# Optimization experiments

Hardware: AMD Instinct MI355X
Metric: run time of the kernel (lower is better)

## Reference

```python
import jax, jax.numpy as jnp
import numpy as np

N_TRAIN, N_FEAT, N_HID, ENC = 4096, 64, 256, 256
N_ANTES, ATT_H, MAX_LEN = 2048, 256, 16


def setup_inputs() -> dict:
    key = jax.random.key(0)
    ks = jax.random.split(key, 8)
    s = 0.05
    f32 = jnp.float32
    return {
        "context": jax.random.normal(ks[0], (N_TRAIN, N_FEAT), f32),
        "S": jax.random.uniform(ks[1], (N_TRAIN, N_ANTES), dtype=f32),
        "enc_w1": s * jax.random.normal(ks[2], (N_HID, N_FEAT), f32),
        "enc_b1": jnp.zeros((N_HID,), f32),
        "enc_w2": s * jax.random.normal(ks[3], (ENC, N_HID), f32),
        "enc_b2": jnp.zeros((ENC,), f32),
        "w_ih": s * jax.random.normal(ks[4], (4 * ENC, N_ANTES), f32),
        "w_hh": s * jax.random.normal(ks[5], (4 * ENC, ENC), f32),
        "b_ih": jnp.zeros((4 * ENC,), f32),
        "b_hh": jnp.zeros((4 * ENC,), f32),
        "att_w1": s * jax.random.normal(ks[6], (ATT_H, N_TRAIN + ENC), f32),
        "att_b1": jnp.zeros((ATT_H,), f32),
        "att_w2": s * jax.random.normal(ks[7], (1, ATT_H), f32),
        "att_b2": jnp.zeros((1,), f32),
    }


def _forward(context, S, enc_w1, enc_b1, enc_w2, enc_b2,
             w_ih, w_hh, b_ih, b_hh, att_w1, att_b1, att_w2, att_b2):
    n_train, n_antes = S.shape
    # context encoder: Linear -> ReLU -> Linear, initializes LSTM hidden state
    phi = jax.nn.relu(context @ enc_w1.T + enc_b1) @ enc_w2.T + enc_b2  # [n_train, ENC]
    # attention first layer split: columns [:n_train] act on S.T rows, rest on e_t
    Wa, Wb = att_w1[:, :n_train], att_w1[:, n_train:]
    pre = S.T @ Wa.T  # [n_antes, ATT_H], constant across timesteps
    bias = b_ih + b_hh
    x0 = jnp.ones((n_train, n_antes), S.dtype)

    def step(carry, _):
        h, c, x = carry
        # one LSTM cell step (PyTorch gate order i, f, g, o)
        z = x @ w_ih.T + h @ w_hh.T + bias  # [n_train, 4*ENC]
        i, f, g, o = jnp.split(z, 4, axis=-1)
        c = jax.nn.sigmoid(f) * c + jax.nn.sigmoid(i) * jnp.tanh(g)
        h = jax.nn.sigmoid(o) * jnp.tanh(c)
        e_t = h.mean(axis=0)  # mean over n_train (torch e.mean(1) on [1,n_train,H])
        hid = jax.nn.relu(pre + e_t @ Wb.T + att_b1)  # [n_antes, ATT_H]
        scores = (hid @ att_w2.T + att_b2)[:, 0]      # [n_antes]
        logp = jax.nn.log_softmax(scores, axis=0)
        idx = jnp.argmax(logp)
        # next input: chosen antecedent column broadcast across all antecedents
        x_next = jnp.broadcast_to(S[:, idx][:, None], (n_train, n_antes))
        return (h, c, x_next), logp

    _, d = jax.lax.scan(jax.checkpoint(step), (phi, jnp.zeros_like(phi), x0),
                        None, length=MAX_LEN)
    return d  # [MAX_LEN, n_antes] == torch cat(...).transpose(0, 1)


def reference(context, S, enc_w1, enc_b1, enc_w2, enc_b2,
              w_ih, w_hh, b_ih, b_hh, att_w1, att_b1, att_w2, att_b2):
    return _forward(context, S, enc_w1, enc_b1, enc_w2, enc_b2,
                    w_ih, w_hh, b_ih, b_hh, att_w1, att_b1, att_w2, att_b2)
```

## Files before the change

### kernel.cpp

```cpp
#include <hip/hip_runtime.h>
#include <hip/hip_bf16.h>
#include <math.h>

#define N_TRAIN 4096
#define N_FEAT  64
#define N_HID   256
#define ENC     256
#define N_ANTES 2048
#define ATT_H   256
#define MAX_LEN 16

typedef unsigned int u32;
typedef unsigned short u16;
typedef short short8 __attribute__((ext_vector_type(8)));
typedef float floatx16 __attribute__((ext_vector_type(16)));

__device__ __forceinline__ float fsig(float x)  { return 1.f / (1.f + __expf(-x)); }
__device__ __forceinline__ float ftanh(float x) { return 2.f / (1.f + __expf(-2.f * x)) - 1.f; }

__device__ __forceinline__ u16 f2bf(float x) {
    u32 b = __float_as_uint(x);
    return (u16)((b + 0x7FFFu + ((b >> 16) & 1u)) >> 16);
}
__device__ __forceinline__ float bf2f(u16 h) {
    return __uint_as_float(((u32)h) << 16);
}
__device__ __forceinline__ void split_bf(float v, u16& hi, u16& lo) {
    u32 b = __float_as_uint(v);
    hi = (u16)(b >> 16);
    float r = v - __uint_as_float(b & 0xFFFF0000u);
    lo = (u16)(__float_as_uint(r) >> 16);
}

__device__ __forceinline__ int kin_of(int l, int j) {
    return ((l >> 5) << 2) + (j & 3) + ((j >> 2) << 3);
}

template <bool RELU>
__global__ __launch_bounds__(256) void gemm_abT(
    const float* __restrict__ A, const float* __restrict__ B,
    const float* __restrict__ bias, float* __restrict__ C,
    int M, int N, int K, int lda, int ldb, int ldc)
{
    __shared__ __align__(16) float As[16][68];
    __shared__ __align__(16) float Bs[16][68];
    const int tid = threadIdx.x;
    const int m0 = blockIdx.x * 64, n0 = blockIdx.y * 64;
    const int tx = tid & 15, ty = tid >> 4;
    const int kl = tid & 15, rl = tid >> 4;
    float acc[4][4] = {};

    for (int k0 = 0; k0 < K; k0 += 16) {
        #pragma unroll
        for (int pp = 0; pp < 4; ++pp) {
            int r = rl + pp * 16;
            As[kl][r] = A[(size_t)(m0 + r) * lda + k0 + kl];
            Bs[kl][r] = B[(size_t)(n0 + r) * ldb + k0 + kl];
        }
        __syncthreads();
        #pragma unroll
        for (int k = 0; k < 16; ++k) {
            float4 av = *(const float4*)&As[k][ty * 4];
            float4 bv = *(const float4*)&Bs[k][tx * 4];
            float a4[4] = {av.x, av.y, av.z, av.w};
            float b4[4] = {bv.x, bv.y, bv.z, bv.w};
            #pragma unroll
            for (int i = 0; i < 4; ++i)
                #pragma unroll
                for (int j = 0; j < 4; ++j)
                    acc[i][j] = fmaf(a4[i], b4[j], acc[i][j]);
        }
        __syncthreads();
    }
    #pragma unroll
    for (int i = 0; i < 4; ++i) {
        int m = m0 + ty * 4 + i;
        #pragma unroll
        for (int j = 0; j < 4; ++j) {
            int n = n0 + tx * 4 + j;
            float v = acc[i][j] + bias[n];
            if (RELU) v = fmaxf(v, 0.f);
            C[(size_t)m * ldc + n] = v;
        }
    }
}

__global__ __launch_bounds__(256) void k_rowsum(const float* __restrict__ w_ih,
                                                float* __restrict__ rowsum)
{
    __shared__ float red[256];
    const int j = blockIdx.x, tid = threadIdx.x;
    float s = 0.f;
    for (int i = tid; i < N_ANTES; i += 256) s += w_ih[(size_t)j * N_ANTES + i];
    red[tid] = s; __syncthreads();
    for (int off = 128; off > 0; off >>= 1) {
        if (tid < off) red[tid] += red[tid + off];
        __syncthreads();
    }
    if (tid == 0) rowsum[j] = red[0];
}

__global__ __launch_bounds__(256) void k_wbT(const float* __restrict__ att_w1,
                                             float* __restrict__ WbT)
{
    int gid = blockIdx.x * 256 + threadIdx.x;
    int j = gid >> 8, k = gid & 255;
    WbT[(size_t)k * 256 + j] = att_w1[(size_t)j * (N_TRAIN + ENC) + N_TRAIN + k];
}

__global__ __launch_bounds__(256) void k_packAf(const float* __restrict__ att_w1,
                                                u16* __restrict__ Af_hi,
                                                u16* __restrict__ Af_lo)
{
    int gid = blockIdx.x * 256 + threadIdx.x;
    int j  = gid & 7;
    int l  = (gid >> 3) & 63;
    int kt = (gid >> 9) & 255;
    int mt = gid >> 17;
    int m = mt * 32 + (l & 31);
    int k = kt * 16 + kin_of(l, j);
    float v = att_w1[(size_t)m * (N_TRAIN + ENC) + k];
    u16 hi, lo; split_bf(v, hi, lo);
    Af_hi[gid] = hi;
    Af_lo[gid] = lo;
}

#define PSPLIT 8
__global__ __launch_bounds__(256) void k_gemm_preT(
    const u16* __restrict__ Af_hi, const u16* __restrict__ Af_lo,
    const float* __restrict__ S, float* __restrict__ P)
{
    const int tid = threadIdx.x, lane = tid & 63, w = tid >> 6;
    const int kz = blockIdx.x;
    const int np = blockIdx.y;
    const int mq = blockIdx.z;
    const int mt = mq * 2 + (w & 1);
    const int ni = w >> 1;
    const int nb = np * 64 + ni * 32 + (lane & 31);
    const int kb = 4 * (lane >> 5);
    floatx16 acc = {0,0,0,0,0,0,0,0,0,0,0,0,0,0,0,0};

    const int kt_beg = kz * 32, kt_end = kt_beg + 32;
    #pragma unroll 4
    for (int kt = kt_beg; kt < kt_end; ++kt) {
        size_t ao = (((size_t)mt * 256 + kt) * 64 + lane) * 8;
        short8 ahi = *(const short8*)(Af_hi + ao);
        short8 alo = *(const short8*)(Af_lo + ao);
        short8 bhi, blo;
        #pragma unroll
        for (int j = 0; j < 8; ++j) {
            int k = kt * 16 + kb + (j & 3) + 8 * (j >> 2);
            float v = S[(size_t)k * N_ANTES + nb];
            u16 hi, lo; split_bf(v, hi, lo);
            bhi[j] = (short)hi;
            blo[j] = (short)lo;
        }
        acc = __builtin_amdgcn_mfma_f32_32x32x16_bf16(ahi, bhi, acc, 0, 0, 0);
        acc = __builtin_amdgcn_mfma_f32_32x32x16_bf16(ahi, blo, acc, 0, 0, 0);
        acc = __builtin_amdgcn_mfma_f32_32x32x16_bf16(alo, bhi, acc, 0, 0, 0);
    }

    float* Pk = P + (size_t)(kz & 3) * (ATT_H * N_ANTES);
    #pragma unroll
    for (int q = 0; q < 16; ++q) {
        int row = mt * 32 + (q & 3) + 8 * (q >> 2) + 4 * (lane >> 5);
        atomicAdd(&Pk[(size_t)row * N_ANTES + nb], acc[q]);
    }
}

__global__ __launch_bounds__(256) void k_reduce4(const float* __restrict__ P,
                                                 float* __restrict__ preT)
{
    int gid = blockIdx.x * 256 + threadIdx.x;
    const int SZ = ATT_H * N_ANTES;
    preT[gid] = (P[gid] + P[gid + SZ]) + (P[gid + 2 * SZ] + P[gid + 3 * SZ]);
}

__global__ __launch_bounds__(256) void k_packWf(const float* __restrict__ w_hh,
                                                u16* __restrict__ Wf_hi,
                                                u16* __restrict__ Wf_lo)
{
    int gid = blockIdx.x * 256 + threadIdx.x;
    int j    = gid & 7;
    int l    = (gid >> 3) & 63;
    int kt   = (gid >> 9) & 15;
    int nsub = (gid >> 13) & 1;
    int cb   = gid >> 14;
    int k  = kt * 16 + kin_of(l, j);
    int cc = nsub * 32 + (l & 31);
    int jj = cb * 16 + (cc >> 2);
    int g  = cc & 3;
    int J  = g * 256 + jj;
    float v = w_hh[(size_t)J * 256 + k];
    u16 hi = f2bf(v);
    Wf_hi[gid] = hi;
    Wf_lo[gid] = f2bf(v - bf2f(hi));
}

__global__ __launch_bounds__(256) void k_packHf(const float* __restrict__ h,
                                                u16* __restrict__ Hf_hi,
                                                u16* __restrict__ Hf_lo)
{
    int gid = blockIdx.x * 256 + threadIdx.x;
    int j  = gid & 7;
    int l  = (gid >> 3) & 63;
    int kt = (gid >> 9) & 15;
    int mt = gid >> 13;
    int m = mt * 32 + (l & 31);
    int k = kt * 16 + kin_of(l, j);
    float v = h[(size_t)m * 256 + k];
    u16 hi = f2bf(v);
    Hf_hi[gid] = hi;
    Hf_lo[gid] = f2bf(v - bf2f(hi));
}

__global__ __launch_bounds__(256) void k_zgemm(
    const u16* __restrict__ Hf_hi_r, const u16* __restrict__ Hf_lo_r,
    u16* __restrict__ Hf_hi_w, u16* __restrict__ Hf_lo_w,
    const u16* __restrict__ Wf_hi, const u16* __restrict__ Wf_lo,
    float* __restrict__ c,
    const float* __restrict__ rowsum, const float* __restrict__ b_ih,
    const float* __restrict__ b_hh, const float* __restrict__ S,
    const int* __restrict__ idx_buf, int t, float* __restrict__ e_acc_t)
{
    __shared__ __align__(16) float z_lds[64][68];
    __shared__ float red[256];
    const int tid  = threadIdx.x;
    const int lane = tid & 63;
    const int w    = tid >> 6;
    const int rb = blockIdx.x;
    const int cb = blockIdx.y;
    const int mt = rb * 2 + (w & 1);
    const int ni = w >> 1;

    floatx16 acc = {0,0,0,0,0,0,0,0,0,0,0,0,0,0,0,0};
    const size_t aoff = (size_t)mt * 16 * 512 + lane * 8;
    const size_t boff = (size_t)(cb * 2 + ni) * 16 * 512 + lane * 8;

    #pragma unroll 4
    for (int kt = 0; kt < 16; ++kt) {
        short8 ahi = *(const short8*)(Hf_hi_r + aoff + kt * 512);
        short8 alo = *(const short8*)(Hf_lo_r + aoff + kt * 512);
        short8 bhi = *(const short8*)(Wf_hi   + boff + kt * 512);
        short8 blo = *(const short8*)(Wf_lo   + boff + kt * 512);
        acc = __builtin_amdgcn_mfma_f32_32x32x16_bf16(ahi, bhi, acc, 0, 0, 0);
        acc = __builtin_amdgcn_mfma_f32_32x32x16_bf16(ahi, blo, acc, 0, 0, 0);
        acc = __builtin_amdgcn_mfma_f32_32x32x16_bf16(alo, bhi, acc, 0, 0, 0);
    }

    #pragma unroll
    for (int q = 0; q < 16; ++q) {
        int row = (w & 1) * 32 + (q & 3) + 8 * (q >> 2) + 4 * (lane >> 5);
        z_lds[row][ni * 32 + (lane & 31)] = acc[q];
    }
    __syncthreads();

    const int jj_l = tid & 15, rg = tid >> 4;
    const int Jc = cb * 16 + jj_l;
    float rs[4], bs[4];
    #pragma unroll
    for (int g = 0; g < 4; ++g) {
        int J = g * 256 + Jc;
        rs[g] = rowsum[J];
        bs[g] = b_ih[J] + b_hh[J];
    }
    const int idxp = (t > 0) ? idx_buf[t - 1] : 0;
    float esum = 0.f;
    #pragma unroll
    for (int p = 0; p < 4; ++p) {
        int r = rg * 4 + p;
        int rglob = rb * 64 + r;
        float a = (t > 0) ? S[(size_t)rglob * N_ANTES + idxp] : 1.f;
        float4 z4 = *(const float4*)&z_lds[r][jj_l * 4];
        float zi = z4.x + fmaf(a, rs[0], bs[0]);
        float zf = z4.y + fmaf(a, rs[1], bs[1]);
        float zg = z4.z + fmaf(a, rs[2], bs[2]);
        float zo = z4.w + fmaf(a, rs[3], bs[3]);
        size_t coff = (size_t)rglob * 256 + Jc;
        float cn = fsig(zf) * c[coff] + fsig(zi) * ftanh(zg);
        float hn = fsig(zo) * ftanh(cn);
        c[coff] = cn;
        esum += hn;
        u16 hi = f2bf(hn);
        u16 lo = f2bf(hn - bf2f(hi));
        int mtw    = rglob >> 5;
        int lane_a = (rglob & 31) + 32 * ((Jc >> 2) & 1);
        int ktw    = Jc >> 4;
        int jw     = (Jc & 3) + ((Jc >> 3) & 1) * 4;
        size_t off = (((size_t)mtw * 16 + ktw) * 64 + lane_a) * 8 + jw;
        Hf_hi_w[off] = hi;
        Hf_lo_w[off] = lo;
    }
    red[tid] = esum;
    __syncthreads();
    if (tid < 16) {
        float s = 0.f;
        #pragma unroll
        for (int q = 0; q < 16; ++q) s += red[tid + q * 16];
        atomicAdd(&e_acc_t[Jc - jj_l + tid], s);
    }
}

__global__ __launch_bounds__(256) void k_att(
    const float* __restrict__ preT, const float* __restrict__ e_accum_t,
    const float* __restrict__ WbT, const float* __restrict__ att_b1,
    const float* __restrict__ att_w2, const float* __restrict__ att_b2,
    float* __restrict__ scores, float* __restrict__ out_t,
    int* __restrict__ idx_t, int* __restrict__ cnt)
{
    __shared__ float e_lds[256];
    __shared__ float u[256];
    __shared__ float w2s[256];
    __shared__ float red[256];
    const int tid = threadIdx.x;
    e_lds[tid] = e_accum_t[tid] * (1.f / (float)N_TRAIN);
    w2s[tid] = att_w2[tid];
    __syncthreads();

    float uacc = att_b1[tid];
    for (int k = 0; k < 256; ++k)
        uacc = fmaf(e_lds[k], WbT[(size_t)k * 256 + tid], uacc);
    u[tid] = uacc;
    __syncthreads();

    const int pl = tid & 31, jq = tid >> 5;
    const int p = blockIdx.x * 32 + pl;
    float sc = 0.f;
    #pragma unroll 4
    for (int j = jq; j < 256; j += 8) {
        float v = preT[(size_t)j * N_ANTES + p] + u[j];
        sc = fmaf(fmaxf(v, 0.f), w2s[j], sc);
    }
    red[tid] = sc;
    __syncthreads();
    if (tid < 32) {
        float s = att_b2[0];
        #pragma unroll
        for (int q = 0; q < 8; ++q) s += red[tid + q * 32];
        scores[blockIdx.x * 32 + tid] = s;
    }

    __threadfence();
    __syncthreads();
    __shared__ int is_last;
    if (tid == 0)
        is_last = (atomicAdd(cnt, 1) == (int)gridDim.x - 1);
    __syncthreads();
    if (!is_last) return;
    __threadfence();

    __shared__ float smax[256];
    __shared__ int   sidx[256];
    __shared__ float ssum[256];

    float sv[8];
    #pragma unroll
    for (int i = 0; i < 8; ++i) sv[i] = scores[tid * 8 + i];

    float lmax = -INFINITY; int lidx = 0;
    #pragma unroll
    for (int i = 0; i < 8; ++i)
        if (sv[i] > lmax) { lmax = sv[i]; lidx = tid * 8 + i; }
    smax[tid] = lmax; sidx[tid] = lidx;
    __syncthreads();
    for (int off = 128; off > 0; off >>= 1) {
        if (tid < off) {
            float ov = smax[tid + off]; int oi = sidx[tid + off];
            if (ov > smax[tid] || (ov == smax[tid] && oi < sidx[tid])) {
                smax[tid] = ov; sidx[tid] = oi;
            }
        }
        __syncthreads();
    }
    const float gmax = smax[0];
    const int gidx = sidx[0];

    float lsum = 0.f;
    #pragma unroll
    for (int i = 0; i < 8; ++i) lsum += __expf(sv[i] - gmax);
    ssum[tid] = lsum;
    __syncthreads();
    for (int off = 128; off > 0; off >>= 1) {
        if (tid < off) ssum[tid] += ssum[tid + off];
        __syncthreads();
    }
    const float lse = gmax + logf(ssum[0]);

    #pragma unroll
    for (int i = 0; i < 8; ++i)
        out_t[tid * 8 + i] = sv[i] - lse;
    if (tid == 0) {
        idx_t[0] = gidx;
        *cnt = 0;
    }
}

extern "C" void kernel_launch(void* const* d_in, const int* in_sizes, int n_in,
                              void* d_out, int out_size, void* d_ws, size_t ws_size,
                              hipStream_t stream)
{
    (void)in_sizes; (void)n_in; (void)out_size; (void)ws_size;
    const float* context = (const float*)d_in[0];
    const float* S       = (const float*)d_in[1];
    const float* enc_w1  = (const float*)d_in[2];
    const float* enc_b1  = (const float*)d_in[3];
    const float* enc_w2  = (const float*)d_in[4];
    const float* enc_b2  = (const float*)d_in[5];
    const float* w_ih    = (const float*)d_in[6];
    const float* w_hh    = (const float*)d_in[7];
    const float* b_ih    = (const float*)d_in[8];
    const float* b_hh    = (const float*)d_in[9];
    const float* att_w1  = (const float*)d_in[10];
    const float* att_b1  = (const float*)d_in[11];
    const float* att_w2  = (const float*)d_in[12];
    const float* att_b2  = (const float*)d_in[13];
    float* out = (float*)d_out;
    float* ws  = (float*)d_ws;

    float* P      = ws;
    float* h_fp32 = ws;
    float* c      = ws + 1048576;
    float* hid1   = ws + 2097152;
    float* preT   = ws + 3145728;
    u16* Af_hi  = (u16*)(ws + 2097152);
    u16* Af_lo  = (u16*)(ws + 2621440);
    u16* Hf_hi1 = (u16*)(ws + 0);
    u16* Hf_lo1 = (u16*)(ws + 524288);
    u16* Hf_hi0 = (u16*)(ws + 2097152);
    u16* Hf_lo0 = (u16*)(ws + 2621440);
    u16* Wf_hi  = (u16*)(ws + 3670016);
    u16* Wf_lo  = (u16*)(ws + 3801088);
    int*   cnt    = (int*)(ws + 4718592);
    float* rowsum = ws + 4984832;
    float* e_acc  = ws + 4985856;
    float* scores = ws + 4989952;
    float* WbT    = ws + 4992000;
    int*   idxbuf = (int*)(ws + 5057536);

    k_rowsum<<<1024, 256, 0, stream>>>(w_ih, rowsum);
    k_wbT<<<256, 256, 0, stream>>>(att_w1, WbT);
    k_packWf<<<1024, 256, 0, stream>>>(w_hh, Wf_hi, Wf_lo);

    k_packAf<<<4096, 256, 0, stream>>>(att_w1, Af_hi, Af_lo);
    hipMemsetAsync(P, 0, (size_t)4 * ATT_H * N_ANTES * sizeof(float), stream);
    dim3 gp(PSPLIT, N_ANTES / 64, 4);
    k_gemm_preT<<<gp, 256, 0, stream>>>(Af_hi, Af_lo, S, P);
    k_reduce4<<<(ATT_H * N_ANTES) / 256, 256, 0, stream>>>(P, preT);

    hipMemsetAsync(c, 0, (size_t)N_TRAIN * ENC * sizeof(float), stream);
    hipMemsetAsync(e_acc, 0, (size_t)MAX_LEN * ENC * sizeof(float), stream);
    hipMemsetAsync(cnt, 0, sizeof(int), stream);

    dim3 g1(N_TRAIN / 64, N_HID / 64);
    gemm_abT<true><<<g1, 256, 0, stream>>>(context, enc_w1, enc_b1, hid1,
                                           N_TRAIN, N_HID, N_FEAT, N_FEAT, N_FEAT, N_HID);
    dim3 g2(N_TRAIN / 64, ENC / 64);
    gemm_abT<false><<<g2, 256, 0, stream>>>(hid1, enc_w2, enc_b2, h_fp32,
                                            N_TRAIN, ENC, N_HID, N_HID, N_HID, ENC);
    k_packHf<<<4096, 256, 0, stream>>>(h_fp32, Hf_hi0, Hf_lo0);

    dim3 gz(64, 16);
    for (int t = 0; t < MAX_LEN; ++t) {
        const u16 *hr, *lr; u16 *hw, *lw;
        if ((t & 1) == 0) { hr = Hf_hi0; lr = Hf_lo0; hw = Hf_hi1; lw = Hf_lo1; }
        else              { hr = Hf_hi1; lr = Hf_lo1; hw = Hf_hi0; lw = Hf_lo0; }
        k_zgemm<<<gz, 256, 0, stream>>>(hr, lr, hw, lw, Wf_hi, Wf_lo, c,
                                        rowsum, b_ih, b_hh, S, idxbuf, t,
                                        e_acc + t * 256);
        k_att<<<N_ANTES / 32, 256, 0, stream>>>(preT, e_acc + t * 256, WbT,
                                                att_b1, att_w2, att_b2, scores,
                                                out + t * N_ANTES, idxbuf + t, cnt);
    }
}
```

Measured before the change: 694.4 us.

## Split zgemm K dimension across waves and double grid rows

The LSTM gate GEMM block now covers 32 rows instead of 64. Its four waves split into two column tiles times two K halves, with the partial sums combined through a doubled LDS buffer in the epilogue. The grid doubles to 128x16 blocks and launch bounds ask for 8 blocks per CU. The aim is more parallelism and occupancy in the per-step recurrent GEMM, at the cost of reloading W tiles across twice as many blocks and an extra LDS reduction.

Result: slower. 716.6 us (+3.2%).

```diff
diff --git a/kernel.cpp b/kernel.cpp
--- a/kernel.cpp
+++ b/kernel.cpp
@@ -214,7 +214,7 @@
     Hf_lo[gid] = f2bf(v - bf2f(hi));
 }
 
-__global__ __launch_bounds__(256) void k_zgemm(
+__global__ __launch_bounds__(256, 8) void k_zgemm(
     const u16* __restrict__ Hf_hi_r, const u16* __restrict__ Hf_lo_r,
     u16* __restrict__ Hf_hi_w, u16* __restrict__ Hf_lo_w,
     const u16* __restrict__ Wf_hi, const u16* __restrict__ Wf_lo,
@@ -223,22 +223,23 @@
     const float* __restrict__ b_hh, const float* __restrict__ S,
     const int* __restrict__ idx_buf, int t, float* __restrict__ e_acc_t)
 {
-    __shared__ __align__(16) float z_lds[64][68];
+    __shared__ __align__(16) float z_lds[2][32][68];
     __shared__ float red[256];
     const int tid  = threadIdx.x;
     const int lane = tid & 63;
     const int w    = tid >> 6;
     const int rb = blockIdx.x;
     const int cb = blockIdx.y;
-    const int mt = rb * 2 + (w & 1);
-    const int ni = w >> 1;
+    const int ni = w & 1;
+    const int kh = w >> 1;
+    const int mt = rb;
 
     floatx16 acc = {0,0,0,0,0,0,0,0,0,0,0,0,0,0,0,0};
     const size_t aoff = (size_t)mt * 16 * 512 + lane * 8;
     const size_t boff = (size_t)(cb * 2 + ni) * 16 * 512 + lane * 8;
 
-    #pragma unroll 4
-    for (int kt = 0; kt < 16; ++kt) {
+    #pragma unroll
+    for (int kt = kh * 8; kt < kh * 8 + 8; ++kt) {
         short8 ahi = *(const short8*)(Hf_hi_r + aoff + kt * 512);
         short8 alo = *(const short8*)(Hf_lo_r + aoff + kt * 512);
         short8 bhi = *(const short8*)(Wf_hi   + boff + kt * 512);
@@ -250,8 +251,8 @@
 
     #pragma unroll
     for (int q = 0; q < 16; ++q) {
-        int row = (w & 1) * 32 + (q & 3) + 8 * (q >> 2) + 4 * (lane >> 5);
-        z_lds[row][ni * 32 + (lane & 31)] = acc[q];
+        int row = (q & 3) + 8 * (q >> 2) + 4 * (lane >> 5);
+        z_lds[kh][row][ni * 32 + (lane & 31)] = acc[q];
     }
     __syncthreads();
 
@@ -267,15 +268,16 @@
     const int idxp = (t > 0) ? idx_buf[t - 1] : 0;
     float esum = 0.f;
     #pragma unroll
-    for (int p = 0; p < 4; ++p) {
-        int r = rg * 4 + p;
-        int rglob = rb * 64 + r;
+    for (int p = 0; p < 2; ++p) {
+        int r = rg * 2 + p;
+        int rglob = rb * 32 + r;
         float a = (t > 0) ? S[(size_t)rglob * N_ANTES + idxp] : 1.f;
-        float4 z4 = *(const float4*)&z_lds[r][jj_l * 4];
-        float zi = z4.x + fmaf(a, rs[0], bs[0]);
-        float zf = z4.y + fmaf(a, rs[1], bs[1]);
-        float zg = z4.z + fmaf(a, rs[2], bs[2]);
-        float zo = z4.w + fmaf(a, rs[3], bs[3]);
+        float4 zA = *(const float4*)&z_lds[0][r][jj_l * 4];
+        float4 zB = *(const float4*)&z_lds[1][r][jj_l * 4];
+        float zi = (zA.x + zB.x) + fmaf(a, rs[0], bs[0]);
+        float zf = (zA.y + zB.y) + fmaf(a, rs[1], bs[1]);
+        float zg = (zA.z + zB.z) + fmaf(a, rs[2], bs[2]);
+        float zo = (zA.w + zB.w) + fmaf(a, rs[3], bs[3]);
         size_t coff = (size_t)rglob * 256 + Jc;
         float cn = fsig(zf) * c[coff] + fsig(zi) * ftanh(zg);
         float hn = fsig(zo) * ftanh(cn);
@@ -297,7 +299,7 @@
         float s = 0.f;
         #pragma unroll
         for (int q = 0; q < 16; ++q) s += red[tid + q * 16];
-        atomicAdd(&e_acc_t[Jc - jj_l + tid], s);
+        atomicAdd(&e_acc_t[cb * 16 + tid], s);
     }
 }
 
@@ -459,7 +461,7 @@
                                             N_TRAIN, ENC, N_HID, N_HID, N_HID, ENC);
     k_packHf<<<4096, 256, 0, stream>>>(h_fp32, Hf_hi0, Hf_lo0);
 
-    dim3 gz(64, 16);
+    dim3 gz(128, 16);
     for (int t = 0; t < MAX_LEN; ++t) {
         const u16 *hr, *lr; u16 *hw, *lw;
         if ((t & 1) == 0) { hr = Hf_hi0; lr = Hf_lo0; hw = Hf_hi1; lw = Hf_lo1; }
```
